# Kernel optimization log

Measured on AMD Instinct MI355X. Metric: run time of the kernel, lower is better.

The kernel has to match this reference:

```python
import jax, jax.numpy as jnp
import numpy as np

B, N, D_IN, D_OUT, H = 262144, 6, 64, 64, 1
DH = D_OUT // H            # per-head feature dim
ALPHA = 0.2                # LeakyReLU negative slope
NEG = -9e15                # mask fill value from the original module


def setup_inputs() -> dict:
    key = jax.random.key(0)
    ks = jax.random.split(key, 9)
    s = 0.15  # ~xavier scale for 64x64
    node = jax.random.normal(ks[0], (B, N, D_IN), dtype=jnp.float32)
    adj = jax.random.randint(ks[1], (N, N), 0, 2, dtype=jnp.int32)
    W0 = jax.random.normal(ks[2], (D_OUT, D_IN), dtype=jnp.float32) * s
    b0 = jax.random.normal(ks[3], (D_OUT,), dtype=jnp.float32) * 0.01
    W1 = jax.random.normal(ks[4], (D_OUT, D_OUT), dtype=jnp.float32) * s
    b1 = jax.random.normal(ks[5], (D_OUT,), dtype=jnp.float32) * 0.01
    W2 = jax.random.normal(ks[6], (D_OUT, D_OUT), dtype=jnp.float32) * s
    b2 = jax.random.normal(ks[7], (D_OUT,), dtype=jnp.float32) * 0.01
    a = jax.random.normal(ks[8], (H, 2 * DH), dtype=jnp.float32) * s
    return {"node": node, "adj": adj, "W0": W0, "b0": b0,
            "W1": W1, "b1": b1, "W2": W2, "b2": b2, "a": a}


def reference(node, adj, W0, b0, W1, b1, W2, b2, a):
    # Three stacked linear projections (as in the original forward)
    x = node @ W0.T + b0          # [B, N, D_OUT]
    x = x @ W1.T + b1
    x = x @ W2.T + b2
    xh = x.reshape(B, N, H, DH)   # [B, N, H, DH]

    # Edge attention logit decomposes: a . [x_i || x_j] = a_src.x_i + a_dst.x_j.
    # Compute densely over the 6x6 node pairs instead of nonzero+gather+scatter;
    # identical math at kept positions, masked positions get -9e15 as original.
    a_src, a_dst = a[:, :DH], a[:, DH:]
    e_src = jnp.einsum('bnhc,hc->bnh', xh, a_src)  # [B, N, H]
    e_dst = jnp.einsum('bnhc,hc->bnh', xh, a_dst)  # [B, N, H]
    z = e_src[:, :, None, :] + e_dst[:, None, :, :]  # [B, i, j, H]
    logits = jnp.where(z >= 0, z, ALPHA * z)         # LeakyReLU(0.2)
    mask = (adj == 1)[None, :, :, None]              # same adj for every batch
    logits = jnp.where(mask, logits, NEG)
    probs = jax.nn.softmax(logits, axis=2)           # softmax over source j

    out = jnp.einsum('bijh,bjhc->bihc', probs, xh)   # aggregate neighbors
    return out.reshape(B, N, H * DH)                 # bConcat=True
```

## Files before the change

### kernel.cpp

```cpp
#include <hip/hip_runtime.h>
#include <stdint.h>

typedef short v8s __attribute__((ext_vector_type(8)));
typedef float v4f __attribute__((ext_vector_type(4)));
typedef uint16_t u16;

#define NB8   32768
#define ALPHA 0.2f
#define NEGV  -9000000000000000.0f

__device__ __forceinline__ uint32_t bf16rne(float f) {
    uint32_t u = __float_as_uint(f);
    return (u + 0x7FFFu + ((u >> 16) & 1u)) >> 16;
}
__device__ __forceinline__ uint32_t pk2(float lo, float hi) {
    return bf16rne(lo) | (bf16rne(hi) << 16);
}

__global__ __launch_bounds__(256) void gat_pre(
    const float* __restrict__ W0, const float* __restrict__ b0,
    const float* __restrict__ W1, const float* __restrict__ b1,
    const float* __restrict__ W2, const float* __restrict__ b2,
    float* __restrict__ bc_out, u16* __restrict__ wcb16)
{
    __shared__ float T[64 * 64];
    __shared__ float tb[64];
    const int t = threadIdx.x;
    for (int s = 0; s < 16; ++s) {
        int idx = t + 256 * s; int i = idx >> 6, j = idx & 63;
        float acc = 0.f;
        for (int k = 0; k < 64; ++k) acc = fmaf(W1[i * 64 + k], W0[k * 64 + j], acc);
        T[idx] = acc;
    }
    if (t < 64) {
        float acc = b1[t];
        for (int k = 0; k < 64; ++k) acc = fmaf(W1[t * 64 + k], b0[k], acc);
        tb[t] = acc;
    }
    __syncthreads();
    for (int s = 0; s < 16; ++s) {
        int idx = t + 256 * s; int i = idx >> 6, j = idx & 63;
        float acc = 0.f;
        for (int k = 0; k < 64; ++k) acc = fmaf(W2[i * 64 + k], T[k * 64 + j], acc);
        wcb16[idx] = (u16)bf16rne(acc);
    }
    if (t < 64) {
        float acc = b2[t];
        for (int k = 0; k < 64; ++k) acc = fmaf(W2[t * 64 + k], tb[k], acc);
        bc_out[t] = acc;
    }
}

__global__ __launch_bounds__(256, 2) void gat_main(
    const float* __restrict__ node, const int* __restrict__ adj,
    const float* __restrict__ a, const float* __restrict__ bc,
    const u16* __restrict__ wcb16, float* __restrict__ out)
{
    __shared__ u16      xtile[4][48 * 64];
    __shared__ float    ebuf2[4][2][48];
    __shared__ uint32_t pbuf[4][48][4];

    const int tid  = threadIdx.x;
    const int w    = tid >> 6;
    const int lane = tid & 63;
    const int a_   = lane & 15;
    const int h    = lane >> 4;

    uint64_t amask = 0ull;
    #pragma unroll 1
    for (int ij = 0; ij < 36; ++ij) amask |= ((uint64_t)(adj[ij] & 1)) << ij;

    v8s Bw[4][2];
    #pragma unroll
    for (int n = 0; n < 4; ++n)
        #pragma unroll
        for (int kt = 0; kt < 2; ++kt)
            Bw[n][kt] = *(const v8s*)(wcb16 + (16 * n + a_) * 64 + 32 * kt + 8 * h);
    float bcl[4], a_s[4], a_d[4];
    #pragma unroll
    for (int n = 0; n < 4; ++n) {
        bcl[n] = bc[16 * n + a_];
        a_s[n] = a[16 * n + a_];
        a_d[n] = a[64 + 16 * n + a_];
    }

    u16*   xt  = &xtile[w][0];
    float* ebs = &ebuf2[w][0][0];
    float* ebd = &ebuf2[w][1][0];

    const int nwaves = (int)((gridDim.x * blockDim.x) >> 6);
    const int wgid   = (int)((blockIdx.x * blockDim.x + tid) >> 6);

    v4f Araw[3][2][2];
    {
        const char* nb = (const char*)node + (size_t)wgid * 12288 + a_ * 256 + h * 32;
        #pragma unroll
        for (int t = 0; t < 3; ++t) {
            const char* bt = nb + t * 4096;
            Araw[t][0][0] = __builtin_nontemporal_load((const v4f*)(bt));
            Araw[t][0][1] = __builtin_nontemporal_load((const v4f*)(bt + 16));
            Araw[t][1][0] = __builtin_nontemporal_load((const v4f*)(bt + 128));
            Araw[t][1][1] = __builtin_nontemporal_load((const v4f*)(bt + 144));
        }
    }

    #pragma unroll 1
    for (int g = wgid; g < NB8; g += nwaves) {
        v8s A[3][2];
        #pragma unroll
        for (int t = 0; t < 3; ++t)
            #pragma unroll
            for (int kt = 0; kt < 2; ++kt) {
                union { uint32_t u[4]; v8s v; } f;
                f.u[0] = pk2(Araw[t][kt][0][0], Araw[t][kt][0][1]);
                f.u[1] = pk2(Araw[t][kt][0][2], Araw[t][kt][0][3]);
                f.u[2] = pk2(Araw[t][kt][1][0], Araw[t][kt][1][1]);
                f.u[3] = pk2(Araw[t][kt][1][2], Araw[t][kt][1][3]);
                A[t][kt] = f.v;
            }
        if (g + nwaves < NB8) {
            const char* nb = (const char*)node + (size_t)(g + nwaves) * 12288 + a_ * 256 + h * 32;
            #pragma unroll
            for (int t = 0; t < 3; ++t) {
                const char* bt = nb + t * 4096;
                Araw[t][0][0] = __builtin_nontemporal_load((const v4f*)(bt));
                Araw[t][0][1] = __builtin_nontemporal_load((const v4f*)(bt + 16));
                Araw[t][1][0] = __builtin_nontemporal_load((const v4f*)(bt + 128));
                Araw[t][1][1] = __builtin_nontemporal_load((const v4f*)(bt + 144));
            }
        }

        #pragma unroll
        for (int t = 0; t < 3; ++t) {
            float es_p[4] = { 0.f, 0.f, 0.f, 0.f };
            float ed_p[4] = { 0.f, 0.f, 0.f, 0.f };
            #pragma unroll
            for (int n = 0; n < 4; ++n) {
                v4f acc = { bcl[n], bcl[n], bcl[n], bcl[n] };
                acc = __builtin_amdgcn_mfma_f32_16x16x32_bf16(A[t][0], Bw[n][0], acc, 0, 0, 0);
                acc = __builtin_amdgcn_mfma_f32_16x16x32_bf16(A[t][1], Bw[n][1], acc, 0, 0, 0);
                uint32_t p01 = pk2(acc[0], acc[1]);
                uint32_t p23 = pk2(acc[2], acc[3]);
                const int cb = (16 * n + a_) ^ (h << 4);
                const int rb = (16 * t + 4 * h) * 64 + cb;
                xt[rb]       = (u16)p01;
                xt[rb + 64]  = (u16)(p01 >> 16);
                xt[rb + 128] = (u16)p23;
                xt[rb + 192] = (u16)(p23 >> 16);
                #pragma unroll
                for (int r = 0; r < 4; ++r) {
                    es_p[r] = fmaf(acc[r], a_s[n], es_p[r]);
                    ed_p[r] = fmaf(acc[r], a_d[n], ed_p[r]);
                }
            }
            #pragma unroll
            for (int r = 0; r < 4; ++r) {
                #pragma unroll
                for (int m = 8; m > 0; m >>= 1) {
                    es_p[r] += __shfl_xor(es_p[r], m, 16);
                    ed_p[r] += __shfl_xor(ed_p[r], m, 16);
                }
            }
            if (a_ == 0) {
                #pragma unroll
                for (int r = 0; r < 4; ++r) ebs[16 * t + 4 * h + r] = es_p[r];
            }
            if (a_ == 1) {
                #pragma unroll
                for (int r = 0; r < 4; ++r) ebd[16 * t + 4 * h + r] = ed_p[r];
            }
        }

        if (lane < 48) {
            const int bb = lane / 6;
            const int i6 = lane - 6 * bb;
            float es = ebs[lane];
            float ed[6];
            #pragma unroll
            for (int k = 0; k < 3; ++k)
                *(float2*)&ed[2 * k] = *(const float2*)(ebd + 6 * bb + 2 * k);
            uint32_t rm = (uint32_t)((amask >> (i6 * 6)) & 63u);
            float l[6];
            #pragma unroll
            for (int j = 0; j < 6; ++j) {
                float z  = es + ed[j];
                float lk = fmaxf(z, ALPHA * z);
                l[j] = (rm & (1u << j)) ? lk : NEGV;
            }
            float mm = fmaxf(fmaxf(fmaxf(l[0], l[1]), fmaxf(l[2], l[3])), fmaxf(l[4], l[5]));
            float p[6]; float sum = 0.f;
            #pragma unroll
            for (int j = 0; j < 6; ++j) { p[j] = __expf(l[j] - mm); sum += p[j]; }
            float inv = 1.0f / sum;
            uint4 pk;
            pk.x = pk2(p[0] * inv, p[1] * inv);
            pk.y = pk2(p[2] * inv, p[3] * inv);
            pk.z = pk2(p[4] * inv, p[5] * inv);
            pk.w = 0u;
            *(uint4*)&pbuf[w][lane][0] = pk;
        }

        {
            const int b = lane >> 3;
            const int q = lane & 7;
            union { uint4 v; u16 s[8]; } xu[6];
            #pragma unroll
            for (int j = 0; j < 6; ++j) {
                int rj = 6 * b + j;
                int cp = (8 * q) ^ ((((rj >> 2) & 3)) << 4);
                xu[j].v = *(const uint4*)(xt + rj * 64 + cp);
            }
            float* dst = out + ((size_t)(g * 8 + b)) * 384 + 8 * q;
            #pragma unroll
            for (int i2 = 0; i2 < 6; ++i2) {
                uint4 pu = *(const uint4*)&pbuf[w][6 * b + i2][0];
                float p[6];
                p[0] = __uint_as_float(pu.x << 16);
                p[1] = __uint_as_float(pu.x & 0xFFFF0000u);
                p[2] = __uint_as_float(pu.y << 16);
                p[3] = __uint_as_float(pu.y & 0xFFFF0000u);
                p[4] = __uint_as_float(pu.z << 16);
                p[5] = __uint_as_float(pu.z & 0xFFFF0000u);
                float o[8];
                #pragma unroll
                for (int c = 0; c < 8; ++c) {
                    float acc0 = p[0] * __uint_as_float(((uint32_t)xu[0].s[c]) << 16);
                    acc0 = fmaf(p[1], __uint_as_float(((uint32_t)xu[1].s[c]) << 16), acc0);
                    acc0 = fmaf(p[2], __uint_as_float(((uint32_t)xu[2].s[c]) << 16), acc0);
                    acc0 = fmaf(p[3], __uint_as_float(((uint32_t)xu[3].s[c]) << 16), acc0);
                    acc0 = fmaf(p[4], __uint_as_float(((uint32_t)xu[4].s[c]) << 16), acc0);
                    acc0 = fmaf(p[5], __uint_as_float(((uint32_t)xu[5].s[c]) << 16), acc0);
                    o[c] = acc0;
                }
                v4f o0 = { o[0], o[1], o[2], o[3] };
                v4f o1 = { o[4], o[5], o[6], o[7] };
                __builtin_nontemporal_store(o0, (v4f*)(dst + i2 * 64));
                __builtin_nontemporal_store(o1, (v4f*)(dst + i2 * 64 + 4));
            }
        }
    }
}

extern "C" void kernel_launch(void* const* d_in, const int* in_sizes, int n_in,
                              void* d_out, int out_size, void* d_ws, size_t ws_size,
                              hipStream_t stream)
{
    const float* node = (const float*)d_in[0];
    const int*   adj  = (const int*)d_in[1];
    const float* W0   = (const float*)d_in[2];
    const float* b0   = (const float*)d_in[3];
    const float* W1   = (const float*)d_in[4];
    const float* b1   = (const float*)d_in[5];
    const float* W2   = (const float*)d_in[6];
    const float* b2   = (const float*)d_in[7];
    const float* a    = (const float*)d_in[8];
    float* outp = (float*)d_out;

    float* wsf   = (float*)d_ws;
    float* bcp   = wsf;
    u16*   wcb16 = (u16*)(wsf + 64);

    gat_pre<<<1, 256, 0, stream>>>(W0, b0, W1, b1, W2, b2, bcp, wcb16);
    gat_main<<<1024, 256, 0, stream>>>(node, adj, a, bcp, wcb16, outp);
}
```

Baseline: 201.8 us.

## Coalesce node loads and stage bf16 A-fragments through swizzled LDS

Node rows are now loaded fully coalesced, with each lane reading consecutive 16-byte chunks of a contiguous 12 KB group, instead of strided per-fragment loads. The values are converted to bf16 and written into the per-wave LDS tile using an XOR swizzle, then read back in MFMA A-fragment layout. The grid also grows from 1024 to 1280 blocks. This trades extra LDS writes and reads, and reuse of the xt buffer, for better global memory coalescing.

```diff
diff --git a/kernel.cpp b/kernel.cpp
--- a/kernel.cpp
+++ b/kernel.cpp
@@ -85,50 +85,47 @@
     }
 
     u16*   xt  = &xtile[w][0];
+    char*  xc  = (char*)xt;
     float* ebs = &ebuf2[w][0][0];
     float* ebd = &ebuf2[w][1][0];
 
     const int nwaves = (int)((gridDim.x * blockDim.x) >> 6);
     const int wgid   = (int)((blockIdx.x * blockDim.x + tid) >> 6);
 
-    v4f Araw[3][2][2];
+    const int h2   = lane >> 4;
+    const int wc_  = (lane & 15) >> 1;
+    const int wofs = (lane & 1) << 3;
+
+    v4f Araw[12];
     {
-        const char* nb = (const char*)node + (size_t)wgid * 12288 + a_ * 256 + h * 32;
-        #pragma unroll
-        for (int t = 0; t < 3; ++t) {
-            const char* bt = nb + t * 4096;
-            Araw[t][0][0] = __builtin_nontemporal_load((const v4f*)(bt));
-            Araw[t][0][1] = __builtin_nontemporal_load((const v4f*)(bt + 16));
-            Araw[t][1][0] = __builtin_nontemporal_load((const v4f*)(bt + 128));
-            Araw[t][1][1] = __builtin_nontemporal_load((const v4f*)(bt + 144));
-        }
+        const float* nb = node + (size_t)wgid * 3072;
+        #pragma unroll
+        for (int m = 0; m < 12; ++m)
+            Araw[m] = __builtin_nontemporal_load((const v4f*)(nb + m * 256 + 4 * lane));
     }
 
     #pragma unroll 1
     for (int g = wgid; g < NB8; g += nwaves) {
+        #pragma unroll
+        for (int m = 0; m < 12; ++m) {
+            uint2 v;
+            v.x = pk2(Araw[m][0], Araw[m][1]);
+            v.y = pk2(Araw[m][2], Araw[m][3]);
+            int r = 4 * m + h2;
+            *(uint2*)(xc + r * 128 + ((wc_ ^ (r & 7)) << 4) + wofs) = v;
+        }
+        if (g + nwaves < NB8) {
+            const float* nb = node + (size_t)(g + nwaves) * 3072;
+            #pragma unroll
+            for (int m = 0; m < 12; ++m)
+                Araw[m] = __builtin_nontemporal_load((const v4f*)(nb + m * 256 + 4 * lane));
+        }
         v8s A[3][2];
         #pragma unroll
         for (int t = 0; t < 3; ++t)
             #pragma unroll
-            for (int kt = 0; kt < 2; ++kt) {
-                union { uint32_t u[4]; v8s v; } f;
-                f.u[0] = pk2(Araw[t][kt][0][0], Araw[t][kt][0][1]);
-                f.u[1] = pk2(Araw[t][kt][0][2], Araw[t][kt][0][3]);
-                f.u[2] = pk2(Araw[t][kt][1][0], Araw[t][kt][1][1]);
-                f.u[3] = pk2(Araw[t][kt][1][2], Araw[t][kt][1][3]);
-                A[t][kt] = f.v;
-            }
-        if (g + nwaves < NB8) {
-            const char* nb = (const char*)node + (size_t)(g + nwaves) * 12288 + a_ * 256 + h * 32;
-            #pragma unroll
-            for (int t = 0; t < 3; ++t) {
-                const char* bt = nb + t * 4096;
-                Araw[t][0][0] = __builtin_nontemporal_load((const v4f*)(bt));
-                Araw[t][0][1] = __builtin_nontemporal_load((const v4f*)(bt + 16));
-                Araw[t][1][0] = __builtin_nontemporal_load((const v4f*)(bt + 128));
-                Araw[t][1][1] = __builtin_nontemporal_load((const v4f*)(bt + 144));
-            }
-        }
+            for (int kt = 0; kt < 2; ++kt)
+                A[t][kt] = *(const v8s*)(xc + (16 * t + a_) * 128 + (((4 * kt + h) ^ (a_ & 7)) << 4));
 
         #pragma unroll
         for (int t = 0; t < 3; ++t) {
@@ -261,5 +258,5 @@
     u16*   wcb16 = (u16*)(wsf + 64);
 
     gat_pre<<<1, 256, 0, stream>>>(W0, b0, W1, b1, W2, b2, bcp, wcb16);
-    gat_main<<<1024, 256, 0, stream>>>(node, adj, a, bcp, wcb16, outp);
-}
+    gat_main<<<1280, 256, 0, stream>>>(node, adj, a, bcp, wcb16, outp);
+}
```

New measurement: 198.3 us. No clear change (-1.7%).
